# Optimization experiments

Measured on AMD Instinct MI355X. Metric: run time of the kernel, lower is better.

The kernel has to match this reference:

```python
import jax, jax.numpy as jnp
import numpy as np

B, S, D, H = 2, 2048, 1024, 16
DK = D // H


def setup_inputs() -> dict:
    key = jax.random.key(0)
    ks = jax.random.split(key, 11)
    scale = jnp.float32(1.0 / np.sqrt(D))
    inp = {
        "query": jax.random.normal(ks[0], (B, S, D), jnp.float32),
        "key": jax.random.normal(ks[1], (B, S, D), jnp.float32),
        "value": jax.random.normal(ks[2], (B, S, D), jnp.float32),
        # causal mask: True = masked (masked_fill semantics), broadcast over batch/heads
        "mask": jnp.triu(jnp.ones((S, S), dtype=bool), k=1)[None, None, :, :],
        "Wq": jax.random.normal(ks[3], (D, D), jnp.float32) * scale,
        "bq": jnp.zeros((D,), jnp.float32),
        "Wk": jax.random.normal(ks[4], (D, D), jnp.float32) * scale,
        "bk": jnp.zeros((D,), jnp.float32),
        "Wv": jax.random.normal(ks[5], (D, D), jnp.float32) * scale,
        "bv": jnp.zeros((D,), jnp.float32),
        "Wo": jax.random.normal(ks[6], (D, D), jnp.float32) * scale,
        "bo": jnp.zeros((D,), jnp.float32),
    }
    return inp


def _split_heads(x):
    # (B, S, D) -> (B, H, S, DK)
    b, s, _ = x.shape
    return x.reshape(b, s, H, DK).transpose(0, 2, 1, 3)


def reference(query, key, value, mask, Wq, bq, Wk, bk, Wv, bv, Wo, bo):
    # nn.Linear: y = x @ W.T + b
    q = _split_heads(query @ Wq.T + bq)
    k = _split_heads(key @ Wk.T + bk)
    v = _split_heads(value @ Wv.T + bv)

    inv_sqrt_dk = jnp.float32(1.0 / np.sqrt(DK))
    scores = jnp.einsum("bhqd,bhkd->bhqk", q, k) * inv_sqrt_dk  # (B,H,S,S)
    scores = jnp.where(mask, jnp.float32(-jnp.inf), scores)
    weights = jax.nn.softmax(scores, axis=-1)
    weights = jnp.nan_to_num(weights, nan=0.0)  # fully-masked rows -> 0

    attn = jnp.einsum("bhqk,bhkd->bhqd", weights, v)  # (B,H,S,DK)
    merged = attn.transpose(0, 2, 1, 3).reshape(B, S, D)  # merge heads
    return merged @ Wo.T + bo
```

## Files before the change

kernel.cpp:

```cpp
#include <hip/hip_runtime.h>


typedef unsigned short u16;
typedef unsigned int u32;
typedef __attribute__((ext_vector_type(8))) __bf16 bf16x8;
typedef __attribute__((ext_vector_type(8))) unsigned short us8;
typedef __attribute__((ext_vector_type(4))) float f32x4;

#define S_LEN 2048
#define D_DIM 1024
#define NH 16
#define DKH 64
#define Mi 1048576ULL

__device__ __forceinline__ u16 f2bf(float f) {
  return __builtin_bit_cast(u16, (__bf16)f);
}
__device__ __forceinline__ bf16x8 ld_frag(const u16* p) {
  us8 v = *(const us8*)p;
  return __builtin_bit_cast(bf16x8, v);
}
__device__ __forceinline__ void gl2lds16(const u16* g, u16* l) {
  __builtin_amdgcn_global_load_lds(
      (__attribute__((address_space(1))) void*)(g),
      (__attribute__((address_space(3))) void*)(l), 16, 0, 0);
}

__global__ __launch_bounds__(256, 1) void cvt_all(
    const float* __restrict__ q, const float* __restrict__ k, const float* __restrict__ v,
    const float* __restrict__ wq, const float* __restrict__ wk,
    const float* __restrict__ wv, const float* __restrict__ wo,
    u16* __restrict__ dst)
{
  size_t e0 = ((size_t)blockIdx.x * 256 + threadIdx.x) * 8;
  const float* s;
  if      (e0 <  4*Mi) s = q  + e0;
  else if (e0 <  8*Mi) s = k  + (e0 - 4*Mi);
  else if (e0 < 12*Mi) s = v  + (e0 - 8*Mi);
  else if (e0 < 13*Mi) s = wq + (e0 - 12*Mi);
  else if (e0 < 14*Mi) s = wk + (e0 - 13*Mi);
  else if (e0 < 15*Mi) s = wv + (e0 - 14*Mi);
  else                 s = wo + (e0 - 15*Mi);
  float4 a = ((const float4*)s)[0];
  float4 b = ((const float4*)s)[1];
  us8 o;
  o[0]=f2bf(a.x); o[1]=f2bf(a.y); o[2]=f2bf(a.z); o[3]=f2bf(a.w);
  o[4]=f2bf(b.x); o[5]=f2bf(b.y); o[6]=f2bf(b.z); o[7]=f2bf(b.w);
  *(us8*)(dst + e0) = o;
}

__global__ __launch_bounds__(256, 1) void gemm_qkv_bb(
    const u16* __restrict__ Aq, const u16* __restrict__ Ak, const u16* __restrict__ Av,
    const u16* __restrict__ Wqb, const u16* __restrict__ Wkb, const u16* __restrict__ Wvb,
    const float* __restrict__ bq, const float* __restrict__ bk, const float* __restrict__ bv,
    u16* __restrict__ Oq, u16* __restrict__ Ok, u16* __restrict__ Ov, float qscale)
{
  const int z = blockIdx.z;
  const u16* A = (z == 0) ? Aq : (z == 1) ? Ak : Av;
  const u16* W = (z == 0) ? Wqb : (z == 1) ? Wkb : Wvb;
  const float* bias = (z == 0) ? bq : (z == 1) ? bk : bv;
  u16* out = (z == 0) ? Oq : (z == 1) ? Ok : Ov;
  const float scale = (z == 0) ? qscale : 1.0f;
  const int K = 1024;

  __shared__ u16 lA[128 * 32];
  __shared__ u16 lB[128 * 32];
  const int t = threadIdx.x;
  const int w = t >> 6, l = t & 63;
  const int mblk = blockIdx.y * 128, nblk = blockIdx.x * 128;
  const int wm = (w & 1) * 64, wn = (w >> 1) * 64;
  const int lr = l & 15, lq = l >> 4;
  const int srow = l >> 2, scol = (l & 3) * 8;

  f32x4 acc[4][4] = {};

  for (int k0 = 0; k0 < K; k0 += 32) {
    __syncthreads();
    #pragma unroll
    for (int r = 0; r < 2; ++r) {
      int grp = r * 4 + w;
      gl2lds16(A + (size_t)(mblk + grp * 16 + srow) * K + k0 + scol, &lA[grp * 512]);
      gl2lds16(W + (size_t)(nblk + grp * 16 + srow) * K + k0 + scol, &lB[grp * 512]);
    }
    __syncthreads();
    bf16x8 aF[4], bF[4];
    #pragma unroll
    for (int mt = 0; mt < 4; ++mt)
      aF[mt] = ld_frag(&lA[(wm + mt * 16 + lr) * 32 + lq * 8]);
    #pragma unroll
    for (int nt = 0; nt < 4; ++nt)
      bF[nt] = ld_frag(&lB[(wn + nt * 16 + lr) * 32 + lq * 8]);
    #pragma unroll
    for (int mt = 0; mt < 4; ++mt)
      #pragma unroll
      for (int nt = 0; nt < 4; ++nt)
        acc[mt][nt] = __builtin_amdgcn_mfma_f32_16x16x32_bf16(aF[mt], bF[nt], acc[mt][nt], 0, 0, 0);
  }

  #pragma unroll
  for (int mt = 0; mt < 4; ++mt)
    #pragma unroll
    for (int nt = 0; nt < 4; ++nt)
      #pragma unroll
      for (int r = 0; r < 4; ++r) {
        int rowg = mblk + wm + mt * 16 + lq * 4 + r;
        int colg = nblk + wn + nt * 16 + lr;
        float v = (acc[mt][nt][r] + bias[colg]) * scale;
        int b = rowg >> 11, s = rowg & 2047;
        int h = colg >> 6, dk = colg & 63;
        if (z != 2)
          out[(((size_t)(b * NH + h)) * S_LEN + s) * DKH + dk] = f2bf(v);
        else
          out[(((size_t)(b * NH + h)) * DKH + dk) * S_LEN + s] = f2bf(v);
      }
}

__global__ __launch_bounds__(256, 1) void gemm_out_bb(
    const u16* __restrict__ A, const u16* __restrict__ W,
    const float* __restrict__ bias, float* __restrict__ out)
{
  const int K = 1024;
  __shared__ u16 lA[128 * 32];
  __shared__ u16 lB[64 * 32];
  const int t = threadIdx.x;
  const int w = t >> 6, l = t & 63;
  const int mblk = blockIdx.y * 128, nblk = blockIdx.x * 64;
  const int wm = (w & 1) * 64, wn = (w >> 1) * 32;
  const int lr = l & 15, lq = l >> 4;
  const int srow = l >> 2, scol = (l & 3) * 8;

  f32x4 acc[4][2] = {};

  for (int k0 = 0; k0 < K; k0 += 32) {
    __syncthreads();
    #pragma unroll
    for (int r = 0; r < 2; ++r) {
      int grp = r * 4 + w;
      gl2lds16(A + (size_t)(mblk + grp * 16 + srow) * K + k0 + scol, &lA[grp * 512]);
    }
    gl2lds16(W + (size_t)(nblk + w * 16 + srow) * K + k0 + scol, &lB[w * 512]);
    __syncthreads();
    bf16x8 aF[4], bF[2];
    #pragma unroll
    for (int mt = 0; mt < 4; ++mt)
      aF[mt] = ld_frag(&lA[(wm + mt * 16 + lr) * 32 + lq * 8]);
    #pragma unroll
    for (int nt = 0; nt < 2; ++nt)
      bF[nt] = ld_frag(&lB[(wn + nt * 16 + lr) * 32 + lq * 8]);
    #pragma unroll
    for (int mt = 0; mt < 4; ++mt)
      #pragma unroll
      for (int nt = 0; nt < 2; ++nt)
        acc[mt][nt] = __builtin_amdgcn_mfma_f32_16x16x32_bf16(aF[mt], bF[nt], acc[mt][nt], 0, 0, 0);
  }

  #pragma unroll
  for (int mt = 0; mt < 4; ++mt)
    #pragma unroll
    for (int nt = 0; nt < 2; ++nt)
      #pragma unroll
      for (int r = 0; r < 4; ++r) {
        int rowg = mblk + wm + mt * 16 + lq * 4 + r;
        int colg = nblk + wn + nt * 16 + lr;
        out[(size_t)rowg * D_DIM + colg] = acc[mt][nt][r] + bias[colg];
      }
}

__global__ __launch_bounds__(256, 1) void attn_fused(
    const u16* __restrict__ Q, const u16* __restrict__ K,
    const u16* __restrict__ Vt, u16* __restrict__ O)
{
  __shared__ u16 lK[2][64 * 64];
  __shared__ u16 lV[2][64 * 64];

  const int idx = blockIdx.x;
  const int s_ = idx >> 8;
  const int r_ = idx & 255;
  const int bh = r_ & 31;
  const int t_ = r_ >> 5;
  const int qt = (s_ == 0) ? t_ : (s_ == 1) ? 31 - t_ : (s_ == 2) ? 8 + t_ : 23 - t_;
  const int b = bh >> 4, h = bh & 15;
  const int t = threadIdx.x;
  const int w = t >> 6, l = t & 63;
  const int lr = l & 15, lq = l >> 4;

  const u16* Qp = Q + (size_t)bh * S_LEN * DKH;
  const u16* Kp = K + (size_t)bh * S_LEN * DKH;
  const u16* Vp = Vt + (size_t)bh * DKH * S_LEN;

  const int srow8 = l >> 3;
  const int schunk = l & 7;

  const int qrow = qt * 64 + w * 16 + lr;
  bf16x8 qf[2];
  qf[0] = ld_frag(Qp + (size_t)qrow * DKH + lq * 8);
  qf[1] = ld_frag(Qp + (size_t)qrow * DKH + 32 + lq * 8);

  f32x4 o[4] = {};
  f32x4 li4 = {};

  #pragma unroll
  for (int r2 = 0; r2 < 2; ++r2) {
    int grp = r2 * 4 + w;
    int row = grp * 8 + srow8;
    int sw = (row & 3) | (((row >> 3) & 1) << 2);
    int c = schunk ^ sw;
    gl2lds16(Kp + (size_t)row * DKH + c * 8, &lK[0][grp * 512]);
    gl2lds16(Vp + (size_t)row * S_LEN + c * 8, &lV[0][grp * 512]);
  }

  for (int kt = 0; kt <= qt; ++kt) {
    const int cur = kt & 1;
    __syncthreads();

    if (kt < qt) {
      #pragma unroll
      for (int r2 = 0; r2 < 2; ++r2) {
        int grp = r2 * 4 + w;
        int row = grp * 8 + srow8;
        int sw = (row & 3) | (((row >> 3) & 1) << 2);
        int c = schunk ^ sw;
        gl2lds16(Kp + (size_t)((kt + 1) * 64 + row) * DKH + c * 8, &lK[cur ^ 1][grp * 512]);
        gl2lds16(Vp + (size_t)row * S_LEN + (kt + 1) * 64 + c * 8, &lV[cur ^ 1][grp * 512]);
      }
    }

    f32x4 st[4] = {};
    #pragma unroll
    for (int ksd = 0; ksd < 2; ++ksd)
      #pragma unroll
      for (int nt = 0; nt < 4; ++nt) {
        int sig = 32 * (nt >> 1) + 8 * (lr >> 2) + 4 * (nt & 1) + (lr & 3);
        int slot = (ksd * 4 + lq) ^ (lr & 7);
        bf16x8 kb = ld_frag(&lK[cur][sig * 64 + slot * 8]);
        st[nt] = __builtin_amdgcn_mfma_f32_16x16x32_bf16(kb, qf[ksd], st[nt], 0, 0, 0);
      }

    float p[4][4];
    const bool diag = (kt == qt);
    const int qloc = w * 16 + lr;
    #pragma unroll
    for (int nt = 0; nt < 4; ++nt)
      #pragma unroll
      for (int r = 0; r < 4; ++r) {
        int kk = 32 * (nt >> 1) + 8 * lq + 4 * (nt & 1) + r;
        float e = exp2f(st[nt][r]);
        p[nt][r] = (diag && kk > qloc) ? 0.0f : e;
        li4[r] += p[nt][r];
      }

    #pragma unroll
    for (int ks = 0; ks < 2; ++ks) {
      us8 av;
      #pragma unroll
      for (int j = 0; j < 4; ++j) {
        av[j] = f2bf(p[2 * ks][j]);
        av[4 + j] = f2bf(p[2 * ks + 1][j]);
      }
      bf16x8 pa = __builtin_bit_cast(bf16x8, av);
      #pragma unroll
      for (int dblk = 0; dblk < 4; ++dblk) {
        int d = dblk * 16 + lr;
        int sw = (d & 3) | (((d >> 3) & 1) << 2);
        int slot = (4 * ks + lq) ^ sw;
        bf16x8 vb = ld_frag(&lV[cur][d * 64 + slot * 8]);
        o[dblk] = __builtin_amdgcn_mfma_f32_16x16x32_bf16(pa, vb, o[dblk], 0, 0, 0);
      }
    }
  }

  float li = li4[0] + li4[1] + li4[2] + li4[3];
  li += __shfl_xor(li, 16);
  li += __shfl_xor(li, 32);
  float ri[4];
  #pragma unroll
  for (int r = 0; r < 4; ++r) ri[r] = 1.0f / __shfl(li, lq * 4 + r);

  const size_t obase = ((size_t)b * S_LEN + qt * 64 + w * 16) * D_DIM + h * DKH;
  #pragma unroll
  for (int dblk = 0; dblk < 4; ++dblk)
    #pragma unroll
    for (int r = 0; r < 4; ++r)
      O[obase + (size_t)(lq * 4 + r) * D_DIM + dblk * 16 + lr] = f2bf(o[dblk][r] * ri[r]);
}

extern "C" void kernel_launch(void* const* d_in, const int* in_sizes, int n_in,
                              void* d_out, int out_size, void* d_ws, size_t ws_size,
                              hipStream_t stream) {
  const float* query = (const float*)d_in[0];
  const float* key   = (const float*)d_in[1];
  const float* value = (const float*)d_in[2];
  const float* Wq = (const float*)d_in[4];
  const float* bq = (const float*)d_in[5];
  const float* Wk = (const float*)d_in[6];
  const float* bk = (const float*)d_in[7];
  const float* Wv = (const float*)d_in[8];
  const float* bv = (const float*)d_in[9];
  const float* Wo = (const float*)d_in[10];
  const float* bo = (const float*)d_in[11];
  float* out = (float*)d_out;

  const float qscale = 0.125f * 1.44269504088896341f;
  dim3 blk(256);

  u16* base = (u16*)d_ws;
  u16* Qb = base;
  u16* Kb = base + 4 * Mi;
  u16* Vb = base + 8 * Mi;

  u16* cvt = base + 12 * Mi;
  u16* qbf = cvt;
  u16* kbf = cvt + 4 * Mi;
  u16* vbf = cvt + 8 * Mi;
  u16* wqb = cvt + 12 * Mi;
  u16* wkb = cvt + 13 * Mi;
  u16* wvb = cvt + 14 * Mi;
  u16* wob = cvt + 15 * Mi;
  u16* Ab  = qbf;

  cvt_all<<<dim3(8192), blk, 0, stream>>>(query, key, value, Wq, Wk, Wv, Wo, cvt);
  gemm_qkv_bb<<<dim3(8, 32, 3), blk, 0, stream>>>(qbf, kbf, vbf, wqb, wkb, wvb,
                                                  bq, bk, bv, Qb, Kb, Vb, qscale);
  attn_fused<<<dim3(1024), blk, 0, stream>>>(Qb, Kb, Vb, Ab);
  gemm_out_bb<<<dim3(16, 32), blk, 0, stream>>>(Ab, wob, bo, out);
}
```

Before: 233.4 us.

## Widen out-proj GEMM K-tile with swizzled LDS and remap blocks across XCDs

The output-projection GEMM now stages 64-wide K slices per iteration with an XOR-swizzled LDS layout. This halves the number of barrier pairs and is meant to avoid LDS bank conflicts on fragment reads. Both the out GEMM and the attention kernel now use a 1-D grid with an XCD-aware block remap: consecutive blocks on each XCD share rows or heads for L2 locality. The attention kernel also pairs short and long causal tiles so work stays balanced. LDS use per block grows, and the remap changes which blocks are co-resident.

```diff
diff --git a/kernel.cpp b/kernel.cpp
--- a/kernel.cpp
+++ b/kernel.cpp
@@ -120,38 +120,50 @@
     const float* __restrict__ bias, float* __restrict__ out)
 {
   const int K = 1024;
-  __shared__ u16 lA[128 * 32];
-  __shared__ u16 lB[64 * 32];
+  __shared__ u16 lA[128 * 64];
+  __shared__ u16 lB[64 * 64];
+  const int bid = blockIdx.x;
+  const int o   = (bid & 7) * 64 + (bid >> 3);
+  const int mblk = (o >> 4) * 128, nblk = (o & 15) * 64;
   const int t = threadIdx.x;
   const int w = t >> 6, l = t & 63;
-  const int mblk = blockIdx.y * 128, nblk = blockIdx.x * 64;
   const int wm = (w & 1) * 64, wn = (w >> 1) * 32;
   const int lr = l & 15, lq = l >> 4;
-  const int srow = l >> 2, scol = (l & 3) * 8;
+  const int srow = l >> 3;
+  const int sgr  = (l & 7) ^ srow;
 
   f32x4 acc[4][2] = {};
 
-  for (int k0 = 0; k0 < K; k0 += 32) {
-    __syncthreads();
-    #pragma unroll
-    for (int r = 0; r < 2; ++r) {
-      int grp = r * 4 + w;
-      gl2lds16(A + (size_t)(mblk + grp * 16 + srow) * K + k0 + scol, &lA[grp * 512]);
-    }
-    gl2lds16(W + (size_t)(nblk + w * 16 + srow) * K + k0 + scol, &lB[w * 512]);
-    __syncthreads();
-    bf16x8 aF[4], bF[2];
-    #pragma unroll
-    for (int mt = 0; mt < 4; ++mt)
-      aF[mt] = ld_frag(&lA[(wm + mt * 16 + lr) * 32 + lq * 8]);
-    #pragma unroll
-    for (int nt = 0; nt < 2; ++nt)
-      bF[nt] = ld_frag(&lB[(wn + nt * 16 + lr) * 32 + lq * 8]);
-    #pragma unroll
-    for (int mt = 0; mt < 4; ++mt)
+  for (int k0 = 0; k0 < K; k0 += 64) {
+    __syncthreads();
+    #pragma unroll
+    for (int i = 0; i < 4; ++i) {
+      int chunk = w * 4 + i;
+      int row = chunk * 8 + srow;
+      gl2lds16(A + (size_t)(mblk + row) * K + k0 + sgr * 8, &lA[chunk * 512]);
+    }
+    #pragma unroll
+    for (int i = 0; i < 2; ++i) {
+      int chunk = w * 2 + i;
+      int row = chunk * 8 + srow;
+      gl2lds16(W + (size_t)(nblk + row) * K + k0 + sgr * 8, &lB[chunk * 512]);
+    }
+    __syncthreads();
+    #pragma unroll
+    for (int kk = 0; kk < 2; ++kk) {
+      bf16x8 aF[4], bF[2];
+      #pragma unroll
+      for (int mt = 0; mt < 4; ++mt)
+        aF[mt] = ld_frag(&lA[(wm + mt * 16 + lr) * 64 + ((kk * 4 + lq) ^ (lr & 7)) * 8]);
       #pragma unroll
       for (int nt = 0; nt < 2; ++nt)
-        acc[mt][nt] = __builtin_amdgcn_mfma_f32_16x16x32_bf16(aF[mt], bF[nt], acc[mt][nt], 0, 0, 0);
+        bF[nt] = ld_frag(&lB[(wn + nt * 16 + lr) * 64 + ((kk * 4 + lq) ^ (lr & 7)) * 8]);
+      #pragma unroll
+      for (int mt = 0; mt < 4; ++mt)
+        #pragma unroll
+        for (int nt = 0; nt < 2; ++nt)
+          acc[mt][nt] = __builtin_amdgcn_mfma_f32_16x16x32_bf16(aF[mt], bF[nt], acc[mt][nt], 0, 0, 0);
+    }
   }
 
   #pragma unroll
@@ -174,11 +186,10 @@
   __shared__ u16 lV[2][64 * 64];
 
   const int idx = blockIdx.x;
-  const int s_ = idx >> 8;
-  const int r_ = idx & 255;
-  const int bh = r_ & 31;
-  const int t_ = r_ >> 5;
-  const int qt = (s_ == 0) ? t_ : (s_ == 1) ? 31 - t_ : (s_ == 2) ? 8 + t_ : 23 - t_;
+  const int o   = (idx & 7) * 128 + (idx >> 3);
+  const int bh  = (o >> 7) * 4 + (o & 3);
+  const int ts  = (o >> 2) & 31;
+  const int qt  = (ts & 1) ? (31 - (ts >> 1)) : (ts >> 1);
   const int b = bh >> 4, h = bh & 15;
   const int t = threadIdx.x;
   const int w = t >> 6, l = t & 63;
@@ -196,7 +207,7 @@
   qf[0] = ld_frag(Qp + (size_t)qrow * DKH + lq * 8);
   qf[1] = ld_frag(Qp + (size_t)qrow * DKH + 32 + lq * 8);
 
-  f32x4 o[4] = {};
+  f32x4 o4[4] = {};
   f32x4 li4 = {};
 
   #pragma unroll
@@ -264,7 +275,7 @@
         int sw = (d & 3) | (((d >> 3) & 1) << 2);
         int slot = (4 * ks + lq) ^ sw;
         bf16x8 vb = ld_frag(&lV[cur][d * 64 + slot * 8]);
-        o[dblk] = __builtin_amdgcn_mfma_f32_16x16x32_bf16(pa, vb, o[dblk], 0, 0, 0);
+        o4[dblk] = __builtin_amdgcn_mfma_f32_16x16x32_bf16(pa, vb, o4[dblk], 0, 0, 0);
       }
     }
   }
@@ -281,7 +292,7 @@
   for (int dblk = 0; dblk < 4; ++dblk)
     #pragma unroll
     for (int r = 0; r < 4; ++r)
-      O[obase + (size_t)(lq * 4 + r) * D_DIM + dblk * 16 + lr] = f2bf(o[dblk][r] * ri[r]);
+      O[obase + (size_t)(lq * 4 + r) * D_DIM + dblk * 16 + lr] = f2bf(o4[dblk][r] * ri[r]);
 }
 
 extern "C" void kernel_launch(void* const* d_in, const int* in_sizes, int n_in,
@@ -322,5 +333,5 @@
   gemm_qkv_bb<<<dim3(8, 32, 3), blk, 0, stream>>>(qbf, kbf, vbf, wqb, wkb, wvb,
                                                   bq, bk, bv, Qb, Kb, Vb, qscale);
   attn_fused<<<dim3(1024), blk, 0, stream>>>(Qb, Kb, Vb, Ab);
-  gemm_out_bb<<<dim3(16, 32), blk, 0, stream>>>(Ab, wob, bo, out);
-}
+  gemm_out_bb<<<dim3(512), blk, 0, stream>>>(Ab, wob, bo, out);
+}
```

After: 235.3 us. No clear change (+0.8%).
